# Kernel tuning notes

Measured on AMD Instinct MI355X. Metric: run time of the kernel, lower is better.

## Reference

```python
import jax, jax.numpy as jnp
import numpy as np

B = 16384        # batch
NDIS = 20        # discrete features
NCONT = 10       # continuous features
VOCAB = 100000   # per-feature vocab size
EMB = 32         # embedding_size
E = 8            # expert_num
T = 2            # task_num
H1, H2 = 512, 256  # expert hidden units
DOUT = 128       # expert_out_dim
TH = 64          # task hidden units
DIN = NDIS * EMB + NCONT  # 650 expert input dim
GIN = NDIS + NCONT        # 30 gate input dim


def setup_inputs() -> dict:
    key = jax.random.key(0)
    ks = jax.random.split(key, 20)
    s = 0.02
    return {
        "X_dis": jax.random.randint(ks[0], (B, NDIS), 0, VOCAB, dtype=jnp.int32),
        "X_cont": jax.random.normal(ks[1], (B, NCONT), dtype=jnp.float32),
        # embedding tables (stacked across the NDIS features)
        "lin_emb": jax.random.normal(ks[2], (NDIS, VOCAB, 1), dtype=jnp.float32) * s,
        "deep_emb": jax.random.normal(ks[3], (NDIS, VOCAB, EMB), dtype=jnp.float32) * s,
        # expert MLPs stacked across experts: 650 -> 512 -> 256 -> 128
        "expert_W1": jax.random.normal(ks[4], (E, DIN, H1), dtype=jnp.float32) * s,
        "expert_b1": jnp.zeros((E, H1), dtype=jnp.float32),
        "expert_W2": jax.random.normal(ks[5], (E, H1, H2), dtype=jnp.float32) * s,
        "expert_b2": jnp.zeros((E, H2), dtype=jnp.float32),
        "expert_W3": jax.random.normal(ks[6], (E, H2, DOUT), dtype=jnp.float32) * s,
        "expert_b3": jnp.zeros((E, DOUT), dtype=jnp.float32),
        # per-task gate: Linear(30 -> E)
        "gate_W": jax.random.normal(ks[7], (T, GIN, E), dtype=jnp.float32) * s,
        "gate_b": jnp.zeros((T, E), dtype=jnp.float32),
        # per-task tower: 128 -> 64 -> 1
        "task_W1": jax.random.normal(ks[8], (T, DOUT, TH), dtype=jnp.float32) * s,
        "task_b1": jnp.zeros((T, TH), dtype=jnp.float32),
        "task_W2": jax.random.normal(ks[9], (T, TH, 1), dtype=jnp.float32) * s,
        "task_b2": jnp.zeros((T, 1), dtype=jnp.float32),
    }


def reference(X_dis, X_cont, lin_emb, deep_emb,
              expert_W1, expert_b1, expert_W2, expert_b2, expert_W3, expert_b3,
              gate_W, gate_b, task_W1, task_b1, task_W2, task_b2):
    fidx = jnp.arange(NDIS)[None, :]                      # [1, NDIS]
    # batched embedding gathers across all discrete features
    lin = lin_emb[fidx, X_dis][..., 0]                    # [B, NDIS]
    deep = deep_emb[fidx, X_dis].reshape(X_dis.shape[0], -1)  # [B, NDIS*EMB]
    expert_in = jnp.concatenate([deep, X_cont], axis=1)   # [B, 650]
    gate_in = jnp.concatenate([lin, X_cont], axis=1)      # [B, 30]

    # grouped expert MLPs
    h = jax.nn.relu(jnp.einsum('bi,eih->beh', expert_in, expert_W1) + expert_b1)
    h = jax.nn.relu(jnp.einsum('beh,eho->beo', h, expert_W2) + expert_b2)
    expert_out = jnp.einsum('beh,ehd->bed', h, expert_W3) + expert_b3  # [B, E, DOUT]

    # per-task softmax gates and weighted combine
    gates = jax.nn.softmax(jnp.einsum('bi,tie->bte', gate_in, gate_W) + gate_b, axis=-1)
    task_in = jnp.einsum('bte,bed->btd', gates, expert_out)            # [B, T, DOUT]

    # task towers
    t = jax.nn.relu(jnp.einsum('btd,tdh->bth', task_in, task_W1) + task_b1)
    out = (jnp.einsum('bth,tho->bto', t, task_W2) + task_b2)[..., 0]   # [B, T]
    return out
```

## Files before the change

kernel.cpp:

```cpp
#include <hip/hip_runtime.h>


typedef unsigned short u16;
typedef unsigned int u32;
typedef __attribute__((ext_vector_type(8))) __bf16 bf16x8;
typedef __attribute__((ext_vector_type(4))) float f32x4;
typedef __attribute__((ext_vector_type(4))) unsigned short u16x4;

#define DEVINL __device__ __forceinline__
#define MFMA16(a, b, c) __builtin_amdgcn_mfma_f32_16x16x32_bf16(a, b, c, 0, 0, 0)

DEVINL u16 f2bf(float f) {
  union { float f; u32 u; } x; x.f = f;
  u32 u = x.u;
  return (u16)((u + 0x7fffu + ((u >> 16) & 1u)) >> 16);
}
DEVINL float bf2f(u16 h) {
  union { u32 u; float f; } x; x.u = ((u32)h) << 16;
  return x.f;
}
DEVINL void gload16(const u16* g, u16* l) {
  __builtin_amdgcn_global_load_lds((const __attribute__((address_space(1))) void*)g,
                                   (__attribute__((address_space(3))) void*)l,
                                   16, 0, 0);
}

__global__ __launch_bounds__(256)
void transpose_w_kernel(const float* __restrict__ W, u16* __restrict__ WT,
                        int K, int N, int Kpad)
{
  __shared__ float tbuf[16][65];
  const int e = blockIdx.z;
  const float* We = W + (size_t)e * K * N;
  u16* Wt = WT + (size_t)e * N * Kpad;
  const int k0 = blockIdx.x * 16, n0 = blockIdx.y * 64;
#pragma unroll
  for (int p = 0; p < 4; ++p) {
    const int idx = threadIdx.x + p * 256;
    const int nl = idx & 63, kl = idx >> 6;
    const int gk = k0 + kl;
    tbuf[kl][nl] = (gk < K) ? We[(size_t)gk * N + n0 + nl] : 0.f;
  }
  __syncthreads();
#pragma unroll
  for (int p = 0; p < 4; ++p) {
    const int idx = threadIdx.x + p * 256;
    const int kl = idx & 15, nl = idx >> 4;
    Wt[(size_t)(n0 + nl) * Kpad + k0 + kl] = f2bf(tbuf[kl][nl]);
  }
}

__global__ __launch_bounds__(256)
void gather_kernel(const int* __restrict__ Xd, const float* __restrict__ Xc,
                   const float* __restrict__ lin_emb, const float* __restrict__ deep_emb,
                   const float* __restrict__ gW, const float* __restrict__ gb,
                   u16* __restrict__ ein, float* __restrict__ gates,
                   int rowBase, int Bc)
{
  __shared__ float gi[4][32];
  const int wid = threadIdx.x >> 6, lane = threadIdx.x & 63;
  const int rl = blockIdx.x * 4 + wid;
  const int r = rowBase + rl;
  const int* xd = Xd + (size_t)r * 20;
  u16* er = ein + (size_t)rl * 704;
#pragma unroll
  for (int i = 0; i < 3; ++i) {
    const int li = i * 64 + lane;
    if (li < 160) {
      const int f = li >> 3, sub = li & 7;
      const int idx = xd[f];
      const float4 v = *(const float4*)&deep_emb[((size_t)f * 100000 + idx) * 32 + sub * 4];
      u16x4 o;
      o.x = f2bf(v.x); o.y = f2bf(v.y); o.z = f2bf(v.z); o.w = f2bf(v.w);
      *(u16x4*)&er[f * 32 + sub * 4] = o;
    }
  }
  if (lane < 10) er[640 + lane] = f2bf(Xc[(size_t)r * 10 + lane]);
  if (lane < 54) er[650 + lane] = 0;
  if (lane < 20) gi[wid][lane] = lin_emb[(size_t)lane * 100000 + xd[lane]];
  if (lane < 10) gi[wid][20 + lane] = Xc[(size_t)r * 10 + lane];
  asm volatile("s_waitcnt lgkmcnt(0)" ::: "memory");
  float logit = 0.f;
  const int t = lane >> 3, ee = lane & 7;
  if (lane < 16) {
    float a = gb[t * 8 + ee];
#pragma unroll
    for (int i = 0; i < 30; ++i) a += gi[wid][i] * gW[(t * 30 + i) * 8 + ee];
    logit = a;
  }
  float mx = logit;
#pragma unroll
  for (int d = 1; d < 8; d <<= 1) mx = fmaxf(mx, __shfl_xor(mx, d));
  float p = expf(logit - mx);
  float sm = p;
#pragma unroll
  for (int d = 1; d < 8; d <<= 1) sm += __shfl_xor(sm, d);
  if (lane < 16) gates[(size_t)rl * 16 + lane] = p / sm;
}

#define AFRAGS(M0, M1)                                                         \
  a00 = *(const bf16x8*)(As0 + (M0) * 1024 + aoff0);                           \
  a01 = *(const bf16x8*)(As0 + (M0) * 1024 + aoff1);                           \
  a10 = *(const bf16x8*)(As0 + (M1) * 1024 + aoff0);                           \
  a11 = *(const bf16x8*)(As0 + (M1) * 1024 + aoff1);

#define SYNC_MFMA(M0, M1)                                                      \
  __builtin_amdgcn_s_barrier();                                                \
  asm volatile("s_waitcnt lgkmcnt(0)" ::: "memory");                           \
  __builtin_amdgcn_sched_barrier(0);                                           \
  __builtin_amdgcn_s_setprio(1);                                               \
  acc[M0][0] = MFMA16(a00, b00, acc[M0][0]);                                   \
  acc[M0][0] = MFMA16(a01, b01, acc[M0][0]);                                   \
  acc[M0][1] = MFMA16(a00, b10, acc[M0][1]);                                   \
  acc[M0][1] = MFMA16(a01, b11, acc[M0][1]);                                   \
  acc[M0][2] = MFMA16(a00, b20, acc[M0][2]);                                   \
  acc[M0][2] = MFMA16(a01, b21, acc[M0][2]);                                   \
  acc[M0][3] = MFMA16(a00, b30, acc[M0][3]);                                   \
  acc[M0][3] = MFMA16(a01, b31, acc[M0][3]);                                   \
  acc[M1][0] = MFMA16(a10, b00, acc[M1][0]);                                   \
  acc[M1][0] = MFMA16(a11, b01, acc[M1][0]);                                   \
  acc[M1][1] = MFMA16(a10, b10, acc[M1][1]);                                   \
  acc[M1][1] = MFMA16(a11, b11, acc[M1][1]);                                   \
  acc[M1][2] = MFMA16(a10, b20, acc[M1][2]);                                   \
  acc[M1][2] = MFMA16(a11, b21, acc[M1][2]);                                   \
  acc[M1][3] = MFMA16(a10, b30, acc[M1][3]);                                   \
  acc[M1][3] = MFMA16(a11, b31, acc[M1][3]);                                   \
  __builtin_amdgcn_s_setprio(0);                                               \
  __builtin_amdgcn_s_barrier();

template<bool RELU, typename CT>
__global__ __launch_bounds__(512, 2)
void gemm8_kernel(const u16* __restrict__ A, size_t sAe,
                  const u16* __restrict__ Bw, size_t sBe,
                  CT* __restrict__ C, size_t sCe, int ldc,
                  const float* __restrict__ bias, int N, int K,
                  int nCol, int nRow)
{
  __shared__ __align__(16) u16 As[2][2][8192];
  __shared__ __align__(16) u16 Bs[2][2][8192];

  const int perE = nCol * nRow;
  const int work = (blockIdx.x & 7) * perE + (blockIdx.x >> 3);
  const int e = work / perE;
  const int rem = work - e * perE;
  const int mt = rem / nCol, ct = rem - mt * nCol;

  const u16* Ae = A + (size_t)e * sAe;
  const u16* Be = Bw + (size_t)e * sBe;
  const int row0 = mt * 256, col0 = ct * 256;
  const int tid = threadIdx.x, lane = tid & 63, wid = tid >> 6;
  const int wr = wid >> 2, wc = wid & 3;
  const int KT = K >> 6;

  const int rA = lane >> 3, ch = lane & 7;
  auto stageA = [&](int buf, int h, int kt) {
    const int kb = kt << 6;
#pragma unroll
    for (int j = 0; j < 2; ++j) {
      const int s = j * 8 + wid;
      const int rr = s * 8 + rA;
      const int gc = ch ^ (rr & 7);
      gload16(Ae + ((size_t)(row0 + h * 128 + rr) * K + kb + (gc << 3)),
              &As[buf][h][s * 512]);
    }
  };
  auto stageB = [&](int buf, int h, int kt) {
    const int kb = kt << 6;
#pragma unroll
    for (int j = 0; j < 2; ++j) {
      const int s = j * 8 + wid;
      const int rr = s * 8 + rA;
      const int gc = ch ^ (rr & 7);
      gload16(Be + ((size_t)(col0 + h * 128 + rr) * K + kb + (gc << 3)),
              &Bs[buf][h][s * 512]);
    }
  };

  const int l15 = lane & 15, l4 = lane >> 4, x0 = lane & 7;
  const int aoff0 = l15 * 64 + ((l4 ^ x0) << 3);
  const int aoff1 = l15 * 64 + (((4 + l4) ^ x0) << 3);
  const int bb = (wc & 1) * 64;
  const int boff0 = (bb + l15) * 64 + ((l4 ^ x0) << 3);
  const int boff1 = (bb + l15) * 64 + (((4 + l4) ^ x0) << 3);

  f32x4 acc[8][4];
#pragma unroll
  for (int m = 0; m < 8; ++m)
#pragma unroll
    for (int n = 0; n < 4; ++n) acc[m][n] = {0.f, 0.f, 0.f, 0.f};

  stageA(0, 0, 0); stageA(0, 1, 0);
  stageB(0, 0, 0); stageB(0, 1, 0);
  if (KT > 1) {
    stageB(1, 0, 1); stageB(1, 1, 1);
    asm volatile("s_waitcnt vmcnt(4)" ::: "memory");
  } else {
    asm volatile("s_waitcnt vmcnt(0)" ::: "memory");
  }
  __builtin_amdgcn_s_barrier();

  for (int u = 0; u < KT; ++u) {
    const int c = u & 1;
    const u16* As0 = &As[c][wr][0];
    const u16* Bs0 = &Bs[c][wc >> 1][0];
    bf16x8 a00, a01, a10, a11;
    bf16x8 b00 = *(const bf16x8*)(Bs0 + 0 * 1024 + boff0);
    bf16x8 b01 = *(const bf16x8*)(Bs0 + 0 * 1024 + boff1);
    bf16x8 b10 = *(const bf16x8*)(Bs0 + 1 * 1024 + boff0);
    bf16x8 b11 = *(const bf16x8*)(Bs0 + 1 * 1024 + boff1);
    bf16x8 b20 = *(const bf16x8*)(Bs0 + 2 * 1024 + boff0);
    bf16x8 b21 = *(const bf16x8*)(Bs0 + 2 * 1024 + boff1);
    bf16x8 b30 = *(const bf16x8*)(Bs0 + 3 * 1024 + boff0);
    bf16x8 b31 = *(const bf16x8*)(Bs0 + 3 * 1024 + boff1);
    AFRAGS(0, 1);
    if (u + 1 < KT) stageA(c ^ 1, 0, u + 1);
    SYNC_MFMA(0, 1);
    AFRAGS(2, 3);
    if (u + 1 < KT) stageA(c ^ 1, 1, u + 1);
    SYNC_MFMA(2, 3);
    AFRAGS(4, 5);
    if (u + 2 < KT) stageB(c, 0, u + 2);
    SYNC_MFMA(4, 5);
    AFRAGS(6, 7);
    if (u + 2 < KT) {
      stageB(c, 1, u + 2);
      asm volatile("s_waitcnt vmcnt(4)" ::: "memory");
    } else {
      asm volatile("s_waitcnt vmcnt(0)" ::: "memory");
    }
    SYNC_MFMA(6, 7);
  }

  const int rl4 = l4 * 4;
#pragma unroll
  for (int n = 0; n < 4; ++n) {
    const int col = col0 + wc * 64 + n * 16 + l15;
    const float bv = bias[(size_t)e * N + col];
#pragma unroll
    for (int m = 0; m < 8; ++m) {
      const int grow = row0 + wr * 128 + m * 16 + rl4;
      CT* cp = C + (size_t)e * sCe + (size_t)grow * ldc + col;
#pragma unroll
      for (int j = 0; j < 4; ++j) {
        float v = acc[m][n][j] + bv;
        if (RELU) v = fmaxf(v, 0.f);
        if constexpr (sizeof(CT) == 2) cp[(size_t)j * ldc] = (CT)f2bf(v);
        else                           cp[(size_t)j * ldc] = (CT)v;
      }
    }
  }
}

template<bool RELU, typename CT>
__global__ __launch_bounds__(256, 2)
void gemm_kernel(const u16* __restrict__ A, size_t sAe,
                 const u16* __restrict__ Bw, size_t sBe,
                 CT* __restrict__ C, size_t sCe, int ldc,
                 const float* __restrict__ bias, int N, int K,
                 int nCol, int nRow)
{
  __shared__ u16 As[2][8192];
  __shared__ u16 Bs[2][8192];

  const int perE = nCol * nRow;
  const int work = (blockIdx.x & 7) * perE + (blockIdx.x >> 3);
  const int e = work / perE;
  const int rem = work - e * perE;
  const int mt = rem / nCol;
  const int ct = rem - mt * nCol;

  const u16* Ae = A + (size_t)e * sAe;
  const u16* Be = Bw + (size_t)e * sBe;
  const int row0 = mt * 128;
  const int col0 = ct * 128;
  const int tid = threadIdx.x;
  const int lane = tid & 63;
  const int wid = tid >> 6;
  const int wr = wid >> 1, wc = wid & 1;

  int rw_[4], gch_[4], ldsOff_[4];
#pragma unroll
  for (int i = 0; i < 4; ++i) {
    const int o = (wid * 4 + i) * 1024 + lane * 16;
    rw_[i] = o >> 7;
    const int ch = (o >> 4) & 7;
    gch_[i] = ch ^ (rw_[i] & 7);
    ldsOff_[i] = (wid * 4 + i) * 512;
  }
  const int KT = K >> 6;

  auto stage = [&](int buf, int kt) {
    const int kb = kt << 6;
#pragma unroll
    for (int i = 0; i < 4; ++i) {
      gload16(Ae + ((size_t)(row0 + rw_[i]) * K + kb + (gch_[i] << 3)),
              &As[buf][ldsOff_[i]]);
      gload16(Be + ((size_t)(col0 + rw_[i]) * K + kb + (gch_[i] << 3)),
              &Bs[buf][ldsOff_[i]]);
    }
  };

  f32x4 acc[4][4];
#pragma unroll
  for (int m = 0; m < 4; ++m)
#pragma unroll
    for (int n = 0; n < 4; ++n) acc[m][n] = {0.f, 0.f, 0.f, 0.f};

  stage(0, 0);
  __syncthreads();

  for (int kt = 0; kt < KT; ++kt) {
    const int cur = kt & 1;
    if (kt + 1 < KT) stage(cur ^ 1, kt + 1);
#pragma unroll
    for (int half = 0; half < 2; ++half) {
      const int kp = half * 4 + (lane >> 4);
      bf16x8 af[4], bfr[4];
#pragma unroll
      for (int m = 0; m < 4; ++m) {
        const int rw = wr * 64 + m * 16 + (lane & 15);
        af[m] = *(const bf16x8*)&As[cur][rw * 64 + ((kp ^ (rw & 7)) << 3)];
      }
#pragma unroll
      for (int n = 0; n < 4; ++n) {
        const int rw = wc * 64 + n * 16 + (lane & 15);
        bfr[n] = *(const bf16x8*)&Bs[cur][rw * 64 + ((kp ^ (rw & 7)) << 3)];
      }
      __builtin_amdgcn_s_setprio(1);
#pragma unroll
      for (int m = 0; m < 4; ++m)
#pragma unroll
        for (int n = 0; n < 4; ++n)
          acc[m][n] = MFMA16(af[m], bfr[n], acc[m][n]);
      __builtin_amdgcn_s_setprio(0);
    }
    __syncthreads();
  }

  const int cl = lane & 15;
  const int rl4 = (lane >> 4) * 4;
#pragma unroll
  for (int n = 0; n < 4; ++n) {
    const int col = col0 + wc * 64 + n * 16 + cl;
    const float bv = bias[(size_t)e * N + col];
#pragma unroll
    for (int m = 0; m < 4; ++m) {
      const int grow = row0 + wr * 64 + m * 16 + rl4;
      CT* cp = C + (size_t)e * sCe + (size_t)grow * ldc + col;
#pragma unroll
      for (int j = 0; j < 4; ++j) {
        float v = acc[m][n][j] + bv;
        if (RELU) v = fmaxf(v, 0.f);
        if constexpr (sizeof(CT) == 2) cp[(size_t)j * ldc] = (CT)f2bf(v);
        else                           cp[(size_t)j * ldc] = (CT)v;
      }
    }
  }
}

__global__ __launch_bounds__(256)
void tower_kernel(const u16* __restrict__ eo,
                  const float* __restrict__ gates,
                  const float* __restrict__ tW1,
                  const float* __restrict__ tb1, const float* __restrict__ tW2,
                  const float* __restrict__ tb2, float* __restrict__ out,
                  int rowBase, int Bc)
{
  __shared__ u16 w1s[2 * 128 * 64];
  __shared__ float tin[4][2][128];
  for (int i = threadIdx.x; i < 2 * 128 * 64; i += 256) w1s[i] = f2bf(tW1[i]);
  __syncthreads();
  const int wid = threadIdx.x >> 6, lane = threadIdx.x & 63;
  const int stride = gridDim.x * 4;
  for (int it = 0; it < 4; ++it) {
    const int r = blockIdx.x * 4 + wid + it * stride;
    const float* gp = gates + (size_t)r * 16;
    float g[16];
#pragma unroll
    for (int i = 0; i < 16; ++i) g[i] = gp[i];
    float t0a = 0.f, t0b = 0.f, t1a = 0.f, t1b = 0.f;
#pragma unroll
    for (int ee = 0; ee < 8; ++ee) {
      const u32 pv = *(const u32*)(eo + ((size_t)ee * Bc + r) * 128 + lane * 2);
      const float a = bf2f((u16)(pv & 0xffff));
      const float b = bf2f((u16)(pv >> 16));
      t0a += g[ee] * a;      t0b += g[ee] * b;
      t1a += g[8 + ee] * a;  t1b += g[8 + ee] * b;
    }
    tin[wid][0][lane * 2] = t0a; tin[wid][0][lane * 2 + 1] = t0b;
    tin[wid][1][lane * 2] = t1a; tin[wid][1][lane * 2 + 1] = t1b;
    asm volatile("s_waitcnt lgkmcnt(0)" ::: "memory");
#pragma unroll
    for (int t = 0; t < 2; ++t) {
      float acc = tb1[t * 64 + lane];
#pragma unroll 8
      for (int d = 0; d < 128; ++d)
        acc += tin[wid][t][d] * bf2f(w1s[(t * 128 + d) * 64 + lane]);
      acc = fmaxf(acc, 0.f);
      float s = acc * tW2[t * 64 + lane];
#pragma unroll
      for (int dd = 1; dd < 64; dd <<= 1) s += __shfl_xor(s, dd);
      if (lane == 0) out[(size_t)(rowBase + r) * 2 + t] = s + tb2[t];
    }
    asm volatile("s_waitcnt lgkmcnt(0)" ::: "memory");
  }
}

extern "C" void kernel_launch(void* const* d_in, const int* in_sizes, int n_in,
                              void* d_out, int out_size, void* d_ws, size_t ws_size,
                              hipStream_t stream) {
  const int*   X_dis   = (const int*)  d_in[0];
  const float* X_cont  = (const float*)d_in[1];
  const float* lin_emb = (const float*)d_in[2];
  const float* deep_emb= (const float*)d_in[3];
  const float* eW1     = (const float*)d_in[4];
  const float* eb1     = (const float*)d_in[5];
  const float* eW2     = (const float*)d_in[6];
  const float* eb2     = (const float*)d_in[7];
  const float* eW3     = (const float*)d_in[8];
  const float* eb3     = (const float*)d_in[9];
  const float* gW      = (const float*)d_in[10];
  const float* gb      = (const float*)d_in[11];
  const float* tW1     = (const float*)d_in[12];
  const float* tb1     = (const float*)d_in[13];
  const float* tW2     = (const float*)d_in[14];
  const float* tb2     = (const float*)d_in[15];
  float* out = (float*)d_out;

  char* ws = (char*)d_ws;
  u16* w1t = (u16*)(ws + 0);
  u16* w2t = (u16*)(ws + 5767168);
  u16* w3t = (u16*)(ws + 7864320);
  const size_t base = 8388608;

  const int B = 16384;
  int NC = 1;
  while (NC < 64 && base + (size_t)(B / NC) * 13760ull > ws_size) NC <<= 1;
  const int Bc = B / NC;

  u16*   ein   = (u16*)  (ws + base);
  float* gates = (float*)(ws + base + (size_t)Bc * 1408);
  u16*   h1    = (u16*)  (ws + base + (size_t)Bc * 1472);
  u16*   h2    = (u16*)  (ws + base + (size_t)Bc * 1472 + (size_t)Bc * 8192);
  u16*   eo    = h1;

  transpose_w_kernel<<<dim3(44, 8, 8), 256, 0, stream>>>(eW1, w1t, 650, 512, 704);
  transpose_w_kernel<<<dim3(32, 4, 8), 256, 0, stream>>>(eW2, w2t, 512, 256, 512);
  transpose_w_kernel<<<dim3(16, 2, 8), 256, 0, stream>>>(eW3, w3t, 256, 128, 256);

  for (int c = 0; c < NC; ++c) {
    const int rowBase = c * Bc;
    const int nRow8 = Bc / 256;
    gather_kernel<<<Bc / 4, 256, 0, stream>>>(X_dis, X_cont, lin_emb, deep_emb,
                                              gW, gb, ein, gates, rowBase, Bc);
    gemm8_kernel<true, u16><<<2 * nRow8 * 8, 512, 0, stream>>>(
        ein, 0,                 w1t, (size_t)512 * 704,
        h1, (size_t)Bc * 512, 512, eb1, 512, 704, 2, nRow8);
    gemm8_kernel<true, u16><<<1 * nRow8 * 8, 512, 0, stream>>>(
        h1, (size_t)Bc * 512,   w2t, (size_t)256 * 512,
        h2, (size_t)Bc * 256, 256, eb2, 256, 512, 1, nRow8);
    gemm_kernel<false, u16><<<1 * (Bc / 128) * 8, 256, 0, stream>>>(
        h2, (size_t)Bc * 256,   w3t, (size_t)128 * 256,
        eo, (size_t)Bc * 128, 128, eb3, 128, 256, 1, Bc / 128);
    tower_kernel<<<Bc / 16, 256, 0, stream>>>(eo, gates, tW1, tb1, tW2, tb2,
                                              out, rowBase, Bc);
  }
}
```

Baseline: 282.3 us.

## Fuse weight transpose into gather, triple-buffer A in gemm8, use 128-tile GEMM2

Folds the three weight-transpose launches and the gather into one prep kernel, dispatching on block index, to save launch overhead. Raises gemm8's A tile buffering from two to three stages, prefetching A two steps ahead, and drops its occupancy hint to one block per CU because the extra LDS no longer fits two. Runs layer 2 on the 256-thread 128x128 gemm_kernel instead of gemm8 to get more blocks. Side effect: the transpose now runs inside the per-chunk loop, so it repeats for every chunk when the batch is split.

Result: faster. 266.2 us (-5.7%).

```diff
diff --git a/kernel.cpp b/kernel.cpp
--- a/kernel.cpp
+++ b/kernel.cpp
@@ -26,40 +26,50 @@
 }
 
 __global__ __launch_bounds__(256)
-void transpose_w_kernel(const float* __restrict__ W, u16* __restrict__ WT,
-                        int K, int N, int Kpad)
+void prep_kernel(const float* __restrict__ W1, const float* __restrict__ W2,
+                 const float* __restrict__ W3,
+                 u16* __restrict__ w1t, u16* __restrict__ w2t, u16* __restrict__ w3t,
+                 const int* __restrict__ Xd, const float* __restrict__ Xc,
+                 const float* __restrict__ lin_emb, const float* __restrict__ deep_emb,
+                 const float* __restrict__ gW, const float* __restrict__ gb,
+                 u16* __restrict__ ein, float* __restrict__ gates,
+                 int rowBase, int Bc)
 {
   __shared__ float tbuf[16][65];
-  const int e = blockIdx.z;
-  const float* We = W + (size_t)e * K * N;
-  u16* Wt = WT + (size_t)e * N * Kpad;
-  const int k0 = blockIdx.x * 16, n0 = blockIdx.y * 64;
-#pragma unroll
-  for (int p = 0; p < 4; ++p) {
-    const int idx = threadIdx.x + p * 256;
-    const int nl = idx & 63, kl = idx >> 6;
-    const int gk = k0 + kl;
-    tbuf[kl][nl] = (gk < K) ? We[(size_t)gk * N + n0 + nl] : 0.f;
-  }
-  __syncthreads();
-#pragma unroll
-  for (int p = 0; p < 4; ++p) {
-    const int idx = threadIdx.x + p * 256;
-    const int kl = idx & 15, nl = idx >> 4;
-    Wt[(size_t)(n0 + nl) * Kpad + k0 + kl] = f2bf(tbuf[kl][nl]);
-  }
-}
-
-__global__ __launch_bounds__(256)
-void gather_kernel(const int* __restrict__ Xd, const float* __restrict__ Xc,
-                   const float* __restrict__ lin_emb, const float* __restrict__ deep_emb,
-                   const float* __restrict__ gW, const float* __restrict__ gb,
-                   u16* __restrict__ ein, float* __restrict__ gates,
-                   int rowBase, int Bc)
-{
   __shared__ float gi[4][32];
+  const int bid = blockIdx.x;
+
+  if (bid < 4096) {
+    const float* W; u16* WT; int K, N, Kpad, e, kx, ny;
+    if (bid < 2816)      { W = W1; WT = w1t; K = 650; N = 512; Kpad = 704;
+                           e = bid / 352; const int t = bid % 352; kx = t % 44; ny = t / 44; }
+    else if (bid < 3840) { W = W2; WT = w2t; K = 512; N = 256; Kpad = 512;
+                           const int t2 = bid - 2816; e = t2 / 128; const int t = t2 % 128; kx = t % 32; ny = t / 32; }
+    else                 { W = W3; WT = w3t; K = 256; N = 128; Kpad = 256;
+                           const int t3 = bid - 3840; e = t3 / 32; const int t = t3 % 32; kx = t % 16; ny = t / 16; }
+    const float* We = W + (size_t)e * K * N;
+    u16* Wt = WT + (size_t)e * N * Kpad;
+    const int k0 = kx * 16, n0 = ny * 64;
+#pragma unroll
+    for (int p = 0; p < 4; ++p) {
+      const int idx = threadIdx.x + p * 256;
+      const int nl = idx & 63, kl = idx >> 6;
+      const int gk = k0 + kl;
+      tbuf[kl][nl] = (gk < K) ? We[(size_t)gk * N + n0 + nl] : 0.f;
+    }
+    __syncthreads();
+#pragma unroll
+    for (int p = 0; p < 4; ++p) {
+      const int idx = threadIdx.x + p * 256;
+      const int kl = idx & 15, nl = idx >> 4;
+      Wt[(size_t)(n0 + nl) * Kpad + k0 + kl] = f2bf(tbuf[kl][nl]);
+    }
+    return;
+  }
+
+  const int gb_ = bid - 4096;
   const int wid = threadIdx.x >> 6, lane = threadIdx.x & 63;
-  const int rl = blockIdx.x * 4 + wid;
+  const int rl = gb_ * 4 + wid;
   const int r = rowBase + rl;
   const int* xd = Xd + (size_t)r * 20;
   u16* er = ein + (size_t)rl * 704;
@@ -129,14 +139,14 @@
   __builtin_amdgcn_s_barrier();
 
 template<bool RELU, typename CT>
-__global__ __launch_bounds__(512, 2)
+__global__ __launch_bounds__(512, 1)
 void gemm8_kernel(const u16* __restrict__ A, size_t sAe,
                   const u16* __restrict__ Bw, size_t sBe,
                   CT* __restrict__ C, size_t sCe, int ldc,
                   const float* __restrict__ bias, int N, int K,
                   int nCol, int nRow)
 {
-  __shared__ __align__(16) u16 As[2][2][8192];
+  __shared__ __align__(16) u16 As[3][2][8192];
   __shared__ __align__(16) u16 Bs[2][2][8192];
 
   const int perE = nCol * nRow;
@@ -189,20 +199,20 @@
 #pragma unroll
     for (int n = 0; n < 4; ++n) acc[m][n] = {0.f, 0.f, 0.f, 0.f};
 
-  stageA(0, 0, 0); stageA(0, 1, 0);
-  stageB(0, 0, 0); stageB(0, 1, 0);
+  stageA(0, 0, 0); stageA(0, 1, 0); stageB(0, 0, 0); stageB(0, 1, 0);
   if (KT > 1) {
-    stageB(1, 0, 1); stageB(1, 1, 1);
-    asm volatile("s_waitcnt vmcnt(4)" ::: "memory");
+    stageA(1, 0, 1); stageA(1, 1, 1); stageB(1, 0, 1); stageB(1, 1, 1);
+    asm volatile("s_waitcnt vmcnt(8)" ::: "memory");
   } else {
     asm volatile("s_waitcnt vmcnt(0)" ::: "memory");
   }
   __builtin_amdgcn_s_barrier();
 
+  int cA = 0, nA = 2;
   for (int u = 0; u < KT; ++u) {
-    const int c = u & 1;
-    const u16* As0 = &As[c][wr][0];
-    const u16* Bs0 = &Bs[c][wc >> 1][0];
+    const int cB = u & 1;
+    const u16* As0 = &As[cA][wr][0];
+    const u16* Bs0 = &Bs[cB][wc >> 1][0];
     bf16x8 a00, a01, a10, a11;
     bf16x8 b00 = *(const bf16x8*)(Bs0 + 0 * 1024 + boff0);
     bf16x8 b01 = *(const bf16x8*)(Bs0 + 0 * 1024 + boff1);
@@ -212,23 +222,26 @@
     bf16x8 b21 = *(const bf16x8*)(Bs0 + 2 * 1024 + boff1);
     bf16x8 b30 = *(const bf16x8*)(Bs0 + 3 * 1024 + boff0);
     bf16x8 b31 = *(const bf16x8*)(Bs0 + 3 * 1024 + boff1);
+    const bool pf = (u + 2 < KT);
     AFRAGS(0, 1);
-    if (u + 1 < KT) stageA(c ^ 1, 0, u + 1);
+    if (pf) stageA(nA, 0, u + 2);
     SYNC_MFMA(0, 1);
     AFRAGS(2, 3);
-    if (u + 1 < KT) stageA(c ^ 1, 1, u + 1);
+    if (pf) stageA(nA, 1, u + 2);
     SYNC_MFMA(2, 3);
     AFRAGS(4, 5);
-    if (u + 2 < KT) stageB(c, 0, u + 2);
+    if (pf) stageB(cB, 0, u + 2);
     SYNC_MFMA(4, 5);
     AFRAGS(6, 7);
-    if (u + 2 < KT) {
-      stageB(c, 1, u + 2);
-      asm volatile("s_waitcnt vmcnt(4)" ::: "memory");
+    if (pf) {
+      stageB(cB, 1, u + 2);
+      asm volatile("s_waitcnt vmcnt(8)" ::: "memory");
     } else {
       asm volatile("s_waitcnt vmcnt(0)" ::: "memory");
     }
     SYNC_MFMA(6, 7);
+    cA = (cA == 2) ? 0 : cA + 1;
+    nA = (nA == 2) ? 0 : nA + 1;
   }
 
   const int rl4 = l4 * 4;
@@ -264,7 +277,7 @@
 
   const int perE = nCol * nRow;
   const int work = (blockIdx.x & 7) * perE + (blockIdx.x >> 3);
-  const int e = work / perE;
+  const int e  = work / perE;
   const int rem = work - e * perE;
   const int mt = rem / nCol;
   const int ct = rem - mt * nCol;
@@ -444,21 +457,19 @@
   u16*   h2    = (u16*)  (ws + base + (size_t)Bc * 1472 + (size_t)Bc * 8192);
   u16*   eo    = h1;
 
-  transpose_w_kernel<<<dim3(44, 8, 8), 256, 0, stream>>>(eW1, w1t, 650, 512, 704);
-  transpose_w_kernel<<<dim3(32, 4, 8), 256, 0, stream>>>(eW2, w2t, 512, 256, 512);
-  transpose_w_kernel<<<dim3(16, 2, 8), 256, 0, stream>>>(eW3, w3t, 256, 128, 256);
-
   for (int c = 0; c < NC; ++c) {
     const int rowBase = c * Bc;
+    const int nRow = Bc / 128;
     const int nRow8 = Bc / 256;
-    gather_kernel<<<Bc / 4, 256, 0, stream>>>(X_dis, X_cont, lin_emb, deep_emb,
-                                              gW, gb, ein, gates, rowBase, Bc);
+    prep_kernel<<<4096 + Bc / 4, 256, 0, stream>>>(
+        eW1, eW2, eW3, w1t, w2t, w3t,
+        X_dis, X_cont, lin_emb, deep_emb, gW, gb, ein, gates, rowBase, Bc);
     gemm8_kernel<true, u16><<<2 * nRow8 * 8, 512, 0, stream>>>(
         ein, 0,                 w1t, (size_t)512 * 704,
         h1, (size_t)Bc * 512, 512, eb1, 512, 704, 2, nRow8);
-    gemm8_kernel<true, u16><<<1 * nRow8 * 8, 512, 0, stream>>>(
+    gemm_kernel<true, u16><<<2 * nRow * 8, 256, 0, stream>>>(
         h1, (size_t)Bc * 512,   w2t, (size_t)256 * 512,
-        h2, (size_t)Bc * 256, 256, eb2, 256, 512, 1, nRow8);
+        h2, (size_t)Bc * 256, 256, eb2, 256, 512, 2, nRow);
     gemm_kernel<false, u16><<<1 * (Bc / 128) * 8, 256, 0, stream>>>(
         h2, (size_t)Bc * 256,   w3t, (size_t)128 * 256,
         eo, (size_t)Bc * 128, 128, eb3, 128, 256, 1, Bc / 128);
```
